# Optimization experiments

Measured on AMD Instinct MI355X. Metric: run time of the kernel, lower is better.

## Reference

```python
import jax, jax.numpy as jnp
import numpy as np

BQ, BP, L, CIN, H1, H2, COUT = 32, 256, 16, 8192, 256, 32, 8192


def _conv_block(x, w1, b1, w2, b2, w3, b3):
    # x: (B, L, H1) -> Conv1d stack over token dim with residual, as in self.convs
    h = jnp.transpose(x, (0, 2, 1))  # (B, H1, L)
    for w, b in ((w1, b1), (w2, b2), (w3, b3)):
        h = jax.lax.conv_general_dilated(h, w, (1,), [(2, 2)],
                                         dimension_numbers=('NCH', 'OIH', 'NCH'))
        h = jax.nn.relu(h + b[None, :, None])
    return jnp.transpose(h, (0, 2, 1)) + x


def setup_inputs() -> dict:
    key = jax.random.key(0)
    ks = jax.random.split(key, 16)
    query_x = (jax.random.uniform(ks[0], (BQ, L, CIN)) < 0.01).astype(jnp.float32)
    poi_x = (jax.random.uniform(ks[1], (BP, L, CIN)) < 0.01).astype(jnp.float32)
    query_loc = jax.random.uniform(ks[2], (BQ, 2)) * 100.0
    poi_loc = jax.random.uniform(ks[3], (BP, 2)) * 100.0
    enc_w = jax.random.normal(ks[4], (H1, CIN)) * 0.02
    conv_w1 = jax.random.normal(ks[5], (H1, H1, 5)) * 0.02
    conv_w2 = jax.random.normal(ks[6], (H1, H1, 5)) * 0.02
    conv_w3 = jax.random.normal(ks[7], (H1, H1, 5)) * 0.02
    conv_b1 = jnp.zeros((H1,), jnp.float32)
    conv_b2 = jnp.zeros((H1,), jnp.float32)
    conv_b3 = jnp.zeros((H1,), jnp.float32)
    dec_w1 = jax.random.normal(ks[8], (H2, 2 * H1)) * 0.05
    dec_b1 = jnp.zeros((H2,), jnp.float32)
    dec_w2 = jax.random.normal(ks[9], (H2, H2)) * 0.1
    dec_b2 = jnp.zeros((H2,), jnp.float32)
    # torch init fills this with 0; use small randn so the path is non-trivial
    dec_w3 = jax.random.normal(ks[10], (COUT, H2)) * 0.01
    a = jnp.asarray(1.0, jnp.float32)
    b = jnp.asarray(0.0, jnp.float32)
    c = jnp.asarray(1.0, jnp.float32)
    d = jnp.asarray(0.0, jnp.float32)
    return dict(query_x=query_x, query_loc=query_loc, poi_x=poi_x, poi_loc=poi_loc,
                enc_w=enc_w, conv_w1=conv_w1, conv_b1=conv_b1, conv_w2=conv_w2,
                conv_b2=conv_b2, conv_w3=conv_w3, conv_b3=conv_b3,
                dec_w1=dec_w1, dec_b1=dec_b1, dec_w2=dec_w2, dec_b2=dec_b2,
                dec_w3=dec_w3, a=a, b=b, c=c, d=d)


def reference(query_x, query_loc, poi_x, poi_loc, enc_w, conv_w1, conv_b1,
              conv_w2, conv_b2, conv_w3, conv_b3, dec_w1, dec_b1, dec_w2,
              dec_b2, dec_w3, a, b, c, d):
    # --- encode ---
    q_h = _conv_block(query_x @ enc_w.T, conv_w1, conv_b1, conv_w2, conv_b2, conv_w3, conv_b3)
    p_h = _conv_block(poi_x @ enc_w.T, conv_w1, conv_b1, conv_w2, conv_b2, conv_w3, conv_b3)
    q_emb = q_h.mean(axis=1)  # (Bq, H1)
    p_emb = p_h.mean(axis=1)  # (Bp, H1)
    # --- bloom masks ---
    q_bloom = jnp.minimum(query_x.sum(axis=1), 1.0)  # (Bq, 8192)
    p_bloom = jnp.minimum(poi_x.sum(axis=1), 1.0)    # (Bp, 8192)
    interaction = q_bloom[:, None, :] * p_bloom[None, :, :]  # (Bq, Bp, 8192)
    q_bits = q_bloom.sum(axis=-1, keepdims=True)             # (Bq, 1)
    # --- pairwise MLP decode ---
    bq, bp = q_emb.shape[0], p_emb.shape[0]
    all_embed = jnp.concatenate([
        jnp.broadcast_to(q_emb[:, None, :], (bq, bp, q_emb.shape[-1])),
        jnp.broadcast_to(p_emb[None, :, :], (bq, bp, p_emb.shape[-1])),
    ], axis=-1)  # (Bq, Bp, 2*H1)
    h = jax.nn.relu(all_embed)
    h = jax.nn.relu(h @ dec_w1.T + dec_b1)
    h = jax.nn.relu(h @ dec_w2.T + dec_b2)
    w = h @ dec_w3.T  # (Bq, Bp, 8192)
    weights = jnp.where(w >= 0, w, w * 0.125) + 1.0  # LeakyReLU(1/8) + 1
    desc_sim = (interaction * weights).sum(axis=-1) / q_bits  # (Bq, Bp)
    # --- geo-distance fusion ---
    dist = jnp.sqrt(((query_loc[:, None, :] - poi_loc[None, :, :]) ** 2).sum(axis=-1))
    mean = desc_sim.mean(axis=-1, keepdims=True)
    std = jnp.std(desc_sim, axis=-1, keepdims=True, ddof=1)  # torch.std is unbiased
    desc_sim = (desc_sim - mean) / (std + 1e-6)
    dist_sim = -jnp.log(dist + 1.0)
    return (c - jax.nn.sigmoid(a * desc_sim + b)) * (dist_sim - d)
```

## Files before the change

### kernel.cpp

```cpp
#include <hip/hip_runtime.h>

#define NB 288
#define NBQ 32
#define NBP 256
#define LTOK 16
#define CIN 8192
#define H1 256
#define H2 32
#define MASKW 256
#define XROW 264
#define IDXCAP 208

typedef __attribute__((ext_vector_type(8))) short short8;
typedef __attribute__((ext_vector_type(4))) float f32x4;

__device__ __forceinline__ unsigned short f2bf(float f) {
    unsigned u = __float_as_uint(f);
    u += 0x7fffu + ((u >> 16) & 1u);
    return (unsigned short)(u >> 16);
}

__global__ __launch_bounds__(256) void k_transpose_pack(const float* __restrict__ w,
                                                        unsigned* __restrict__ wtp) {
    __shared__ float tile[32][33];
    int k0 = blockIdx.x * 32;
    int h0 = blockIdx.y * 32;
    int tx = threadIdx.x & 31, ty = threadIdx.x >> 5;
#pragma unroll
    for (int i = 0; i < 32; i += 8)
        tile[ty + i][tx] = w[(h0 + ty + i) * CIN + k0 + tx];
    __syncthreads();
    int kl = threadIdx.x >> 3, pw = threadIdx.x & 7;
#pragma unroll
    for (int u = 0; u < 2; ++u) {
        int p = pw + u * 8;
        unsigned lo = f2bf(tile[2 * p][kl]);
        unsigned hi = f2bf(tile[2 * p + 1][kl]);
        wtp[(size_t)(k0 + kl) * 128 + (h0 >> 1) + p] = (hi << 16) | lo;
    }
}

__global__ __launch_bounds__(256) void k_wprep(const float* __restrict__ w1,
                                               const float* __restrict__ w2,
                                               const float* __restrict__ w3,
                                               unsigned short* __restrict__ wtb,
                                               unsigned* __restrict__ wtp) {
    int bx = blockIdx.x;
    if (bx == 0 && threadIdx.x < 128) wtp[(size_t)8192 * 128 + threadIdx.x] = 0;
    int l = bx / 1280;
    int r = bx - l * 1280;
    int o = r / 5;
    int d = r - o * 5;
    int i = threadIdx.x;
    const float* w = (l == 0) ? w1 : (l == 1) ? w2 : w3;
    wtb[(size_t)l * 327680 + (size_t)o * 1280 + d * 256 + i] =
        f2bf(w[(size_t)o * 1280 + i * 5 + d]);
}

__global__ __launch_bounds__(256) void k_scan(const float* __restrict__ qx,
                                              const float* __restrict__ px,
                                              int* __restrict__ idxl,
                                              int* __restrict__ cnts,
                                              unsigned* __restrict__ masks) {
    int row = blockIdx.x;
    int b = row >> 4;
    const float* x = (b < NBQ) ? (qx + (size_t)row * CIN)
                               : (px + (size_t)(row - NBQ * LTOK) * CIN);
    __shared__ int cnt;
    int tid = threadIdx.x;
    if (tid == 0) cnt = 0;
    __syncthreads();
    int* il = idxl + (size_t)row * IDXCAP;
    const float4* x4 = (const float4*)x;
#pragma unroll
    for (int j = 0; j < 8; ++j) {
        float4 v = x4[j * 256 + tid];
        unsigned ox = __float_as_uint(v.x) | __float_as_uint(v.y) |
                      __float_as_uint(v.z) | __float_as_uint(v.w);
        if (ox) {
            int base = (j * 256 + tid) * 4;
            float vv[4] = {v.x, v.y, v.z, v.w};
#pragma unroll
            for (int c = 0; c < 4; ++c) {
                if (vv[c] != 0.f) {
                    int k = base + c;
                    int p = atomicAdd(&cnt, 1);
                    if (p < 192) il[p] = k;
                    atomicOr(&masks[b * MASKW + (k >> 5)], 1u << (k & 31));
                }
            }
        }
    }
    __syncthreads();
    int n = min(cnt, 192);
    if (tid == 0) cnts[row] = n;
    for (int i = n + tid; i < 200; i += 256) il[i] = 8192;
}

__global__ __launch_bounds__(128) void k_gather(const unsigned* __restrict__ wtp,
                                                const int* __restrict__ idxl,
                                                const int* __restrict__ cnts,
                                                float* __restrict__ encoded,
                                                unsigned* __restrict__ xbufu) {
    int row = blockIdx.x, tid = threadIdx.x;
    int n = cnts[row];
    const int* il = idxl + (size_t)row * IDXCAP;
    float aL = 0.f, aH = 0.f;
    for (int j = 0; j < n; j += 8) {
        int4 ia = *(const int4*)(il + j);
        int4 ib = *(const int4*)(il + j + 4);
        int id[8] = {ia.x, ia.y, ia.z, ia.w, ib.x, ib.y, ib.z, ib.w};
#pragma unroll
        for (int u = 0; u < 8; ++u) {
            unsigned v = wtp[(size_t)id[u] * 128 + tid];
            aL += __uint_as_float(v << 16);
            aH += __uint_as_float(v & 0xffff0000u);
        }
    }
    ((float2*)encoded)[(size_t)row * 128 + tid] = float2{aL, aH};
    unsigned bl = f2bf(aL), bh = f2bf(aH);
    xbufu[(size_t)row * 128 + tid] = (bh << 16) | bl;
}

__global__ __launch_bounds__(256) void k_qbits(const unsigned* __restrict__ masks,
                                               float* __restrict__ qbits) {
    __shared__ int red[256];
    int q = blockIdx.x, tid = threadIdx.x;
    red[tid] = __popc(masks[q * MASKW + tid]);
    __syncthreads();
    for (int st = 128; st > 0; st >>= 1) {
        if (tid < st) red[tid] += red[tid + st];
        __syncthreads();
    }
    if (tid == 0) qbits[q] = (float)red[0];
}

__global__ __launch_bounds__(256) void k_cgemm(const unsigned short* __restrict__ actIn,
                                               unsigned short* __restrict__ actOut,
                                               float* __restrict__ actOutF,
                                               const unsigned short* __restrict__ wl,
                                               const float* __restrict__ bias,
                                               int last) {
    __shared__ unsigned short Als[2 * 20 * XROW];
    __shared__ unsigned short Bls[32 * XROW];
    int tid = threadIdx.x;
    int m0 = blockIdx.x * 32, n0 = blockIdx.y * 32;

    int* Ai = (int*)Als;
#pragma unroll
    for (int i = tid; i < 20 * XROW; i += 256) Ai[i] = 0;
    __syncthreads();

    int row = tid >> 3, part = tid & 7;
    {
        const short8* src = (const short8*)(actIn + (size_t)(m0 + row) * 256 + part * 32);
        unsigned short* dst = Als + ((row >> 4) * 20 + (row & 15) + 2) * XROW + part * 32;
#pragma unroll
        for (int j = 0; j < 4; ++j) *(short8*)(dst + j * 8) = src[j];
    }
    const unsigned short* bsrc = wl + (size_t)(n0 + row) * 1280 + part * 32;
    short8 rb[4];
#pragma unroll
    for (int j = 0; j < 4; ++j) rb[j] = *(const short8*)(bsrc + j * 8);

    int lane = tid & 63, wave = tid >> 6;
    int lane15 = lane & 15, quad = lane >> 4;
    int wm = wave & 1, wn = wave >> 1;
    unsigned short* bdst = Bls + row * XROW + part * 32;

    f32x4 acc = (f32x4){0.f, 0.f, 0.f, 0.f};

#pragma unroll 1
    for (int d = 0; d < 5; ++d) {
#pragma unroll
        for (int j = 0; j < 4; ++j) *(short8*)(bdst + j * 8) = rb[j];
        __syncthreads();
        if (d < 4) {
            const unsigned short* s2 = bsrc + (d + 1) * 256;
#pragma unroll
            for (int j = 0; j < 4; ++j) rb[j] = *(const short8*)(s2 + j * 8);
        }
        const unsigned short* ap = Als + (wm * 20 + lane15 + d) * XROW + quad * 8;
        const unsigned short* bp = Bls + (wn * 16 + lane15) * XROW + quad * 8;
#pragma unroll
        for (int kk = 0; kk < 8; ++kk) {
            short8 av = *(const short8*)(ap + kk * 32);
            short8 bv = *(const short8*)(bp + kk * 32);
            acc = __builtin_amdgcn_mfma_f32_16x16x32_bf16(av, bv, acc, 0, 0, 0);
        }
        __syncthreads();
    }

    int o = n0 + wn * 16 + lane15;
    float bv = bias[o];
    int rbase = m0 + wm * 16 + quad * 4;
#pragma unroll
    for (int r = 0; r < 4; ++r) {
        float v = fmaxf(acc[r] + bv, 0.f);
        if (last) actOutF[(size_t)(rbase + r) * 256 + o] = v;
        else      actOut[(size_t)(rbase + r) * 256 + o] = f2bf(v);
    }
}

__global__ __launch_bounds__(256) void k_ab(const float* __restrict__ actF,
                                            const float* __restrict__ encoded,
                                            const float* __restrict__ w1,
                                            float* __restrict__ Cmat) {
    int b = blockIdx.x, tid = threadIdx.x;
    __shared__ float e[256];
    __shared__ float red[256];
    float s = 0.f;
#pragma unroll
    for (int t = 0; t < 16; ++t)
        s += actF[((size_t)b * 16 + t) * 256 + tid] + encoded[((size_t)b * 16 + t) * 256 + tid];
    e[tid] = fmaxf(s * (1.f / 16.f), 0.f);
    __syncthreads();
    int o = tid & 31, seg = tid >> 5;
    const float* wr = w1 + (size_t)o * 512 + (b < NBQ ? 0 : 256) + seg * 32;
    float v = 0.f;
#pragma unroll
    for (int i = 0; i < 32; ++i) v = fmaf(wr[i], e[seg * 32 + i], v);
    red[tid] = v; __syncthreads();
    if (tid < 128) red[tid] += red[tid + 128]; __syncthreads();
    if (tid < 64)  red[tid] += red[tid + 64];  __syncthreads();
    if (tid < 32) {
        red[tid] += red[tid + 32];
        Cmat[b * 32 + tid] = red[tid];
    }
}

__global__ __launch_bounds__(256) void k_pair(const float* __restrict__ Cmat,
                                              const float* __restrict__ b1,
                                              const float* __restrict__ w2,
                                              const float* __restrict__ b2,
                                              const float* __restrict__ w3,
                                              const unsigned* __restrict__ masks,
                                              const float* __restrict__ qbits,
                                              float* __restrict__ desc) {
    int p = blockIdx.x, q = blockIdx.y;
    __shared__ float h1[32];
    __shared__ __align__(16) float h2s[32];
    __shared__ int idxs[3072];
    __shared__ int cnt;
    __shared__ float wsum[4];
    int tid = threadIdx.x;
    if (tid == 0) cnt = 0;
    __syncthreads();
    unsigned m = masks[q * MASKW + tid] & masks[(NBQ + p) * MASKW + tid];
    int nb = __popc(m);
    if (nb) {
        int pos = atomicAdd(&cnt, nb);
        while (m) {
            int bit = __ffs(m) - 1;
            m &= m - 1;
            idxs[pos++] = tid * 32 + bit;
        }
    }
    if (tid < 32)
        h1[tid] = fmaxf(Cmat[q * 32 + tid] + Cmat[(NBQ + p) * 32 + tid] + b1[tid], 0.f);
    __syncthreads();
    if (tid < 32) {
        float s = b2[tid];
#pragma unroll
        for (int j = 0; j < 32; ++j) s = fmaf(w2[tid * 32 + j], h1[j], s);
        h2s[tid] = fmaxf(s, 0.f);
    }
    __syncthreads();
    int n = cnt;
    int rowi = tid >> 3, part = tid & 7;
    float4 h = ((const float4*)h2s)[part];
    float local = 0.f;
    for (int base = 0; base < n; base += 32) {
        int r = base + rowi;
        bool act = r < n;
        float dot = 0.f;
        if (act) {
            float4 wv = *(const float4*)(w3 + (size_t)idxs[r] * 32 + part * 4);
            dot = wv.x * h.x + wv.y * h.y + wv.z * h.z + wv.w * h.w;
        }
        dot += __shfl_xor(dot, 1);
        dot += __shfl_xor(dot, 2);
        dot += __shfl_xor(dot, 4);
        if (act && part == 0)
            local += 1.f + (dot >= 0.f ? dot : dot * 0.125f);
    }
#pragma unroll
    for (int st = 1; st < 64; st <<= 1) local += __shfl_xor(local, st);
    if ((tid & 63) == 0) wsum[tid >> 6] = local;
    __syncthreads();
    if (tid == 0)
        desc[q * 256 + p] = (wsum[0] + wsum[1] + wsum[2] + wsum[3]) / qbits[q];
}

__global__ __launch_bounds__(256) void k_final(const float* __restrict__ desc,
                                               const float* __restrict__ qloc,
                                               const float* __restrict__ ploc,
                                               const float* __restrict__ sa,
                                               const float* __restrict__ sb,
                                               const float* __restrict__ sc,
                                               const float* __restrict__ sd,
                                               float* __restrict__ out) {
    __shared__ float red[256];
    int q = blockIdx.x, tid = threadIdx.x;
    float v = desc[q * 256 + tid];
    red[tid] = v; __syncthreads();
    for (int st = 128; st > 0; st >>= 1) {
        if (tid < st) red[tid] += red[tid + st];
        __syncthreads();
    }
    float mean = red[0] * (1.f / 256.f);
    __syncthreads();
    float dv = v - mean;
    red[tid] = dv * dv; __syncthreads();
    for (int st = 128; st > 0; st >>= 1) {
        if (tid < st) red[tid] += red[tid + st];
        __syncthreads();
    }
    float var = red[0] * (1.f / 255.f);
    float norm = dv / (sqrtf(var) + 1e-6f);
    float dx = qloc[q * 2]     - ploc[tid * 2];
    float dy = qloc[q * 2 + 1] - ploc[tid * 2 + 1];
    float dist = sqrtf(dx * dx + dy * dy);
    float z = sa[0] * norm + sb[0];
    float sig = 1.f / (1.f + expf(-z));
    out[q * 256 + tid] = (sc[0] - sig) * (-logf(dist + 1.f) - sd[0]);
}

extern "C" void kernel_launch(void* const* d_in, const int* in_sizes, int n_in,
                              void* d_out, int out_size, void* d_ws, size_t ws_size,
                              hipStream_t stream) {
    const float* qx   = (const float*)d_in[0];
    const float* qloc = (const float*)d_in[1];
    const float* px   = (const float*)d_in[2];
    const float* ploc = (const float*)d_in[3];
    const float* encw = (const float*)d_in[4];
    const float* cw1  = (const float*)d_in[5];
    const float* cb1  = (const float*)d_in[6];
    const float* cw2  = (const float*)d_in[7];
    const float* cb2  = (const float*)d_in[8];
    const float* cw3  = (const float*)d_in[9];
    const float* cb3  = (const float*)d_in[10];
    const float* dw1  = (const float*)d_in[11];
    const float* db1  = (const float*)d_in[12];
    const float* dw2  = (const float*)d_in[13];
    const float* db2  = (const float*)d_in[14];
    const float* dw3  = (const float*)d_in[15];
    const float* sa   = (const float*)d_in[16];
    const float* sb   = (const float*)d_in[17];
    const float* sc   = (const float*)d_in[18];
    const float* sd   = (const float*)d_in[19];

    char* w = (char*)d_ws;
    unsigned*       wtp     = (unsigned*)w;       w += (size_t)8193 * 128 * 4;
    float*          encoded = (float*)w;          w += (size_t)NB * LTOK * H1 * 4;
    unsigned short* xbuf    = (unsigned short*)w; w += (size_t)NB * LTOK * H1 * 2;
    unsigned short* act1    = (unsigned short*)w; w += (size_t)NB * LTOK * H1 * 2;
    unsigned short* act2    = (unsigned short*)w; w += (size_t)NB * LTOK * H1 * 2;
    float*          actF    = (float*)w;          w += (size_t)NB * LTOK * H1 * 4;
    unsigned short* wtb     = (unsigned short*)w; w += (size_t)3 * 256 * 1280 * 2;
    int*            idxl    = (int*)w;            w += (size_t)NB * LTOK * IDXCAP * 4;
    int*            cnts    = (int*)w;            w += (size_t)NB * LTOK * 4;
    float*          Cmat    = (float*)w;          w += (size_t)NB * H2 * 4;
    unsigned*       masks   = (unsigned*)w;       w += (size_t)NB * MASKW * 4;
    float*          qbits   = (float*)w;          w += 1024;
    float*          desc    = (float*)w;          w += (size_t)NBQ * NBP * 4;

    hipMemsetAsync(masks, 0, (size_t)NB * MASKW * 4, stream);
    k_transpose_pack<<<dim3(CIN / 32, H1 / 32), 256, 0, stream>>>(encw, wtp);
    k_wprep<<<3840, 256, 0, stream>>>(cw1, cw2, cw3, wtb, wtp);
    k_scan<<<NB * LTOK, 256, 0, stream>>>(qx, px, idxl, cnts, masks);
    k_gather<<<NB * LTOK, 128, 0, stream>>>(wtp, idxl, cnts, encoded, (unsigned*)xbuf);
    k_qbits<<<NBQ, 256, 0, stream>>>(masks, qbits);
    dim3 cgrid(NB * LTOK / 32, 8);
    k_cgemm<<<cgrid, 256, 0, stream>>>(xbuf, act1, actF, wtb,              cb1, 0);
    k_cgemm<<<cgrid, 256, 0, stream>>>(act1, act2, actF, wtb + 327680,     cb2, 0);
    k_cgemm<<<cgrid, 256, 0, stream>>>(act2, act1, actF, wtb + 2 * 327680, cb3, 1);
    k_ab<<<NB, 256, 0, stream>>>(actF, encoded, dw1, Cmat);
    k_pair<<<dim3(NBP, NBQ), 256, 0, stream>>>(Cmat, db1, dw2, db2, dw3, masks, qbits, desc);
    k_final<<<NBQ, 256, 0, stream>>>(desc, qloc, ploc, sa, sb, sc, sd, (float*)d_out);
}
```

Measured before the change: 359.2 us.

## Pack dec_w3 to bf16, fold qbits into k_pair, batch scan loads

Adds a kernel that packs dec_w3 rows into bf16 pairs, so each gathered row in k_pair is 64 bytes instead of 128. k_pair now processes 64 rows per iteration with 4 lanes per row. The separate qbits kernel is removed and the popcount of the query mask is reduced inside k_pair. k_scan issues all eight float4 loads up front before processing them. The bf16 weights reduce precision of the weighting term, and an extra small pack kernel is launched each call.

Measured after the change: 351.2 us. 1.02x faster.

```diff
diff --git a/kernel.cpp b/kernel.cpp
--- a/kernel.cpp
+++ b/kernel.cpp
@@ -57,6 +57,15 @@
         f2bf(w[(size_t)o * 1280 + i * 5 + d]);
 }
 
+__global__ __launch_bounds__(256) void k_w3pack(const float* __restrict__ w3,
+                                                unsigned* __restrict__ w3p) {
+    int idx = blockIdx.x * 256 + threadIdx.x;
+    int k = idx >> 4, pw = idx & 15;
+    unsigned lo = f2bf(w3[k * 32 + 2 * pw]);
+    unsigned hi = f2bf(w3[k * 32 + 2 * pw + 1]);
+    w3p[idx] = (hi << 16) | lo;
+}
+
 __global__ __launch_bounds__(256) void k_scan(const float* __restrict__ qx,
                                               const float* __restrict__ px,
                                               int* __restrict__ idxl,
@@ -70,16 +79,18 @@
     int tid = threadIdx.x;
     if (tid == 0) cnt = 0;
     __syncthreads();
+    const float4* x4 = (const float4*)x;
+    float4 r[8];
+#pragma unroll
+    for (int j = 0; j < 8; ++j) r[j] = x4[j * 256 + tid];
     int* il = idxl + (size_t)row * IDXCAP;
-    const float4* x4 = (const float4*)x;
 #pragma unroll
     for (int j = 0; j < 8; ++j) {
-        float4 v = x4[j * 256 + tid];
-        unsigned ox = __float_as_uint(v.x) | __float_as_uint(v.y) |
-                      __float_as_uint(v.z) | __float_as_uint(v.w);
+        unsigned ox = __float_as_uint(r[j].x) | __float_as_uint(r[j].y) |
+                      __float_as_uint(r[j].z) | __float_as_uint(r[j].w);
         if (ox) {
             int base = (j * 256 + tid) * 4;
-            float vv[4] = {v.x, v.y, v.z, v.w};
+            float vv[4] = {r[j].x, r[j].y, r[j].z, r[j].w};
 #pragma unroll
             for (int c = 0; c < 4; ++c) {
                 if (vv[c] != 0.f) {
@@ -122,19 +133,6 @@
     xbufu[(size_t)row * 128 + tid] = (bh << 16) | bl;
 }
 
-__global__ __launch_bounds__(256) void k_qbits(const unsigned* __restrict__ masks,
-                                               float* __restrict__ qbits) {
-    __shared__ int red[256];
-    int q = blockIdx.x, tid = threadIdx.x;
-    red[tid] = __popc(masks[q * MASKW + tid]);
-    __syncthreads();
-    for (int st = 128; st > 0; st >>= 1) {
-        if (tid < st) red[tid] += red[tid + st];
-        __syncthreads();
-    }
-    if (tid == 0) qbits[q] = (float)red[0];
-}
-
 __global__ __launch_bounds__(256) void k_cgemm(const unsigned short* __restrict__ actIn,
                                                unsigned short* __restrict__ actOut,
                                                float* __restrict__ actOutF,
@@ -233,20 +231,20 @@
                                               const float* __restrict__ b1,
                                               const float* __restrict__ w2,
                                               const float* __restrict__ b2,
-                                              const float* __restrict__ w3,
+                                              const unsigned* __restrict__ w3p,
                                               const unsigned* __restrict__ masks,
-                                              const float* __restrict__ qbits,
                                               float* __restrict__ desc) {
     int p = blockIdx.x, q = blockIdx.y;
     __shared__ float h1[32];
     __shared__ __align__(16) float h2s[32];
     __shared__ int idxs[3072];
     __shared__ int cnt;
-    __shared__ float wsum[4];
+    __shared__ float wsum[4], wq[4];
     int tid = threadIdx.x;
     if (tid == 0) cnt = 0;
     __syncthreads();
-    unsigned m = masks[q * MASKW + tid] & masks[(NBQ + p) * MASKW + tid];
+    unsigned mq = masks[q * MASKW + tid];
+    unsigned m = mq & masks[(NBQ + p) * MASKW + tid];
     int nb = __popc(m);
     if (nb) {
         int pos = atomicAdd(&cnt, nb);
@@ -267,29 +265,42 @@
     }
     __syncthreads();
     int n = cnt;
-    int rowi = tid >> 3, part = tid & 7;
-    float4 h = ((const float4*)h2s)[part];
+    int rowi = tid >> 2, part = tid & 3;
+    float h2v[8];
+#pragma unroll
+    for (int j = 0; j < 8; ++j) h2v[j] = h2s[part * 8 + j];
     float local = 0.f;
-    for (int base = 0; base < n; base += 32) {
+    for (int base = 0; base < n; base += 64) {
         int r = base + rowi;
         bool act = r < n;
         float dot = 0.f;
         if (act) {
-            float4 wv = *(const float4*)(w3 + (size_t)idxs[r] * 32 + part * 4);
-            dot = wv.x * h.x + wv.y * h.y + wv.z * h.z + wv.w * h.w;
+            uint4 wv = *(const uint4*)(w3p + (size_t)idxs[r] * 16 + part * 4);
+            unsigned wu[4] = {wv.x, wv.y, wv.z, wv.w};
+#pragma unroll
+            for (int u = 0; u < 4; ++u) {
+                dot += __uint_as_float(wu[u] << 16) * h2v[2 * u];
+                dot += __uint_as_float(wu[u] & 0xffff0000u) * h2v[2 * u + 1];
+            }
         }
         dot += __shfl_xor(dot, 1);
         dot += __shfl_xor(dot, 2);
-        dot += __shfl_xor(dot, 4);
         if (act && part == 0)
             local += 1.f + (dot >= 0.f ? dot : dot * 0.125f);
     }
-#pragma unroll
-    for (int st = 1; st < 64; st <<= 1) local += __shfl_xor(local, st);
-    if ((tid & 63) == 0) wsum[tid >> 6] = local;
-    __syncthreads();
-    if (tid == 0)
-        desc[q * 256 + p] = (wsum[0] + wsum[1] + wsum[2] + wsum[3]) / qbits[q];
+    float qcf = (float)__popc(mq);
+#pragma unroll
+    for (int st = 1; st < 64; st <<= 1) {
+        local += __shfl_xor(local, st);
+        qcf   += __shfl_xor(qcf, st);
+    }
+    if ((tid & 63) == 0) { wsum[tid >> 6] = local; wq[tid >> 6] = qcf; }
+    __syncthreads();
+    if (tid == 0) {
+        float t  = wsum[0] + wsum[1] + wsum[2] + wsum[3];
+        float qb = wq[0] + wq[1] + wq[2] + wq[3];
+        desc[q * 256 + p] = t / qb;
+    }
 }
 
 __global__ __launch_bounds__(256) void k_final(const float* __restrict__ desc,
@@ -358,24 +369,24 @@
     unsigned short* act2    = (unsigned short*)w; w += (size_t)NB * LTOK * H1 * 2;
     float*          actF    = (float*)w;          w += (size_t)NB * LTOK * H1 * 4;
     unsigned short* wtb     = (unsigned short*)w; w += (size_t)3 * 256 * 1280 * 2;
+    unsigned*       w3p     = (unsigned*)w;       w += (size_t)CIN * 16 * 4;
     int*            idxl    = (int*)w;            w += (size_t)NB * LTOK * IDXCAP * 4;
     int*            cnts    = (int*)w;            w += (size_t)NB * LTOK * 4;
     float*          Cmat    = (float*)w;          w += (size_t)NB * H2 * 4;
     unsigned*       masks   = (unsigned*)w;       w += (size_t)NB * MASKW * 4;
-    float*          qbits   = (float*)w;          w += 1024;
     float*          desc    = (float*)w;          w += (size_t)NBQ * NBP * 4;
 
     hipMemsetAsync(masks, 0, (size_t)NB * MASKW * 4, stream);
     k_transpose_pack<<<dim3(CIN / 32, H1 / 32), 256, 0, stream>>>(encw, wtp);
     k_wprep<<<3840, 256, 0, stream>>>(cw1, cw2, cw3, wtb, wtp);
+    k_w3pack<<<512, 256, 0, stream>>>(dw3, w3p);
     k_scan<<<NB * LTOK, 256, 0, stream>>>(qx, px, idxl, cnts, masks);
     k_gather<<<NB * LTOK, 128, 0, stream>>>(wtp, idxl, cnts, encoded, (unsigned*)xbuf);
-    k_qbits<<<NBQ, 256, 0, stream>>>(masks, qbits);
     dim3 cgrid(NB * LTOK / 32, 8);
     k_cgemm<<<cgrid, 256, 0, stream>>>(xbuf, act1, actF, wtb,              cb1, 0);
     k_cgemm<<<cgrid, 256, 0, stream>>>(act1, act2, actF, wtb + 327680,     cb2, 0);
     k_cgemm<<<cgrid, 256, 0, stream>>>(act2, act1, actF, wtb + 2 * 327680, cb3, 1);
     k_ab<<<NB, 256, 0, stream>>>(actF, encoded, dw1, Cmat);
-    k_pair<<<dim3(NBP, NBQ), 256, 0, stream>>>(Cmat, db1, dw2, db2, dw3, masks, qbits, desc);
+    k_pair<<<dim3(NBP, NBQ), 256, 0, stream>>>(Cmat, db1, dw2, db2, w3p, masks, desc);
     k_final<<<NBQ, 256, 0, stream>>>(desc, qloc, ploc, sa, sb, sc, sd, (float*)d_out);
 }
```
